# Kernel optimization log

Hardware: AMD Instinct MI355X
Metric: run time of the kernel (lower is better)

Reference implementation:

```python
import jax, jax.numpy as jnp
import numpy as np

EPS = 1e-09


def _glorot(key, shape):
    fan_in, fan_out = shape[-2], shape[-1]
    std = (2.0 / (fan_in + fan_out)) ** 0.5
    return jax.random.normal(key, shape, dtype=jnp.float32) * std


def setup_inputs() -> dict:
    key = jax.random.key(0)
    kx, k1, k2, k3, k4 = jax.random.split(key, 5)
    B, S, D = 2, 1024, 256
    H, K = 8, 32  # key_dim_frac = 1/8
    return {
        "x": jax.random.normal(kx, (B, S, D), dtype=jnp.float32),
        "Wks": _glorot(k1, (H, D, K)),
        "Wqs": _glorot(k2, (H, D, K)),
        "Wvs": _glorot(k3, (H, D, D)),
        "Wo": _glorot(k4, (H, D, D)),
    }


def reference(x, Wks, Wqs, Wvs, Wo):
    # Per-head projections: [H, B, S, K] / [H, B, S, D]
    keys = jnp.einsum('bsd,hdk->hbsk', x, Wks)
    queries = jnp.einsum('bsd,hdk->hbsk', x, Wqs)
    values = jnp.einsum('bsd,hde->hbse', x, Wvs)

    # Feature map: elu + 1 (strictly positive)
    keys = jax.nn.elu(keys) + 1.0
    queries = jax.nn.elu(queries) + 1.0

    # Auxiliary pairwise attention map [H, B, S, S], causal-masked, row-normalized
    att = jnp.einsum('hbsk,hbtk->hbst', queries, keys)
    S = att.shape[-1]
    causal = jnp.tril(jnp.ones((S, S), dtype=att.dtype))
    att = att * causal
    att = att / (jnp.sum(att, axis=-1, keepdims=True) + EPS)

    # Causal linear attention via cumulative sums of outer products
    # [H, B, S, D, K] cumulative state (memory-bound, mirrors tf.cumsum)
    kv = jnp.einsum('hbsk,hbsd->hbsdk', keys, values)
    kv_cum = jnp.cumsum(kv, axis=2)
    numerator = jnp.einsum('hbsdk,hbsk->hbsd', kv_cum, queries)
    denominator = jnp.einsum('hbsk,hbsk->hbs', jnp.cumsum(keys, axis=2), queries)
    node = numerator / (denominator[..., None] + EPS)

    # Output projection, summed over heads: [B, S, D]
    out = jnp.einsum('hbsd,hde->bse', node, Wo)
    return (out, att)
```

## Files before the change

### kernel.cpp

```cpp
#include <hip/hip_runtime.h>
#include <hip/hip_bf16.h>
#include <cstdio>

#define PB 2
#define PS 1024
#define PD 256
#define PK 32
#define PH 8
#define HB (PH*PB)
#define BS (PB*PS)
#define EPS 1e-9f

typedef __attribute__((ext_vector_type(8))) short bf16x8;
typedef __attribute__((ext_vector_type(4))) float f32x4;

__device__ inline unsigned short f2bf(float f) {
    __hip_bfloat16 h = __float2bfloat16(f);
    return *reinterpret_cast<unsigned short*>(&h);
}

__global__ void k_xb(const float* __restrict__ x, unsigned short* __restrict__ xb) {
    int i = blockIdx.x*256 + threadIdx.x;
    float4 v = ((const float4*)x)[i];
    ushort4 o = {f2bf(v.x), f2bf(v.y), f2bf(v.z), f2bf(v.w)};
    ((ushort4*)xb)[i] = o;
}

__global__ void k_transpose_qk(const float* __restrict__ Wqs, const float* __restrict__ Wks,
                               unsigned short* __restrict__ WqT, unsigned short* __restrict__ WkT) {
    int h = blockIdx.x;
    const float* S = (blockIdx.y ? Wks : Wqs) + (size_t)h*8192;
    unsigned short* D = (blockIdx.y ? WkT : WqT) + (size_t)h*8192;
    __shared__ float T[256*33];
    int tid = threadIdx.x;
#pragma unroll
    for (int p = 0; p < 32; ++p) {
        int idx = p*256 + tid;
        T[(idx>>5)*33 + (idx&31)] = S[idx];
    }
    __syncthreads();
#pragma unroll
    for (int p = 0; p < 8; ++p) {
        int o4 = p*256 + tid;
        int kk = o4 >> 6, d = (o4 & 63)*4;
        ushort4 o;
        o.x = f2bf(T[(d+0)*33 + kk]); o.y = f2bf(T[(d+1)*33 + kk]);
        o.z = f2bf(T[(d+2)*33 + kk]); o.w = f2bf(T[(d+3)*33 + kk]);
        *(ushort4*)(D + (size_t)kk*256 + d) = o;
    }
}

__global__ void k_transpose256(const float* __restrict__ src, unsigned short* __restrict__ dst,
                               int dst_row_stride, int dst_head_stride) {
    int e0 = blockIdx.x*64, d0 = blockIdx.y*64, h = blockIdx.z;
    __shared__ float T[64][69];
    const float* S = src + (size_t)h*65536;
    int ty = threadIdx.x>>4, c4 = threadIdx.x&15;
#pragma unroll
    for (int p = 0; p < 4; ++p) {
        int r = p*16 + ty;
        float4 v = *(const float4*)(S + (size_t)(d0+r)*256 + e0 + c4*4);
        T[r][c4*4+0]=v.x; T[r][c4*4+1]=v.y; T[r][c4*4+2]=v.z; T[r][c4*4+3]=v.w;
    }
    __syncthreads();
    unsigned short* D = dst + (size_t)h*dst_head_stride;
#pragma unroll
    for (int p = 0; p < 4; ++p) {
        int er = p*16 + ty;
        ushort4 o;
        o.x = f2bf(T[c4*4+0][er]); o.y = f2bf(T[c4*4+1][er]);
        o.z = f2bf(T[c4*4+2][er]); o.w = f2bf(T[c4*4+3][er]);
        *(ushort4*)(D + (size_t)(e0+er)*dst_row_stride + d0 + c4*4) = o;
    }
}

__global__ __launch_bounds__(256) void k_proj_qk_mfma(
    const unsigned short* __restrict__ xb, const unsigned short* __restrict__ WqT,
    const unsigned short* __restrict__ WkT,
    float* __restrict__ Q, float* __restrict__ Kf,
    unsigned short* __restrict__ Qb, unsigned short* __restrict__ Kb)
{
    int m0 = blockIdx.x*64;
    int isK = blockIdx.y;
    int n0 = blockIdx.z*64;
    const unsigned short* W = isK ? WkT : WqT;
    int tid = threadIdx.x, w = tid>>6, l15 = tid&15, g = (tid>>4)&3;
    f32x4 zf = {0.f,0.f,0.f,0.f};
    f32x4 acc[4] = {zf,zf,zf,zf};
    const unsigned short* arow = xb + (size_t)(m0+16*w+l15)*256 + 8*g;
#pragma unroll
    for (int kk = 0; kk < 8; ++kk) {
        bf16x8 af = *(const bf16x8*)(arow + kk*32);
#pragma unroll
        for (int nt = 0; nt < 4; ++nt) {
            bf16x8 bf = *(const bf16x8*)(W + (size_t)(n0+16*nt+l15)*256 + kk*32 + 8*g);
            acc[nt] = __builtin_amdgcn_mfma_f32_16x16x32_bf16(af, bf, acc[nt], 0, 0, 0);
        }
    }
    int bs_base = m0 + 16*w + 4*g;
#pragma unroll
    for (int nt = 0; nt < 4; ++nt) {
        int col = n0 + 16*nt + l15;
        int h = col>>5, kk = col&31;
#pragma unroll
        for (int j = 0; j < 4; ++j) {
            int bs = bs_base + j;
            int b = bs>>10, s = bs&1023;
            float z = acc[nt][j];
            z = z > 0.f ? z + 1.f : expf(z);
            size_t idx = ((size_t)(h*PB+b)*PS + s)*PK + kk;
            if (isK) { Kf[idx] = z; Kb[idx] = f2bf(z); }
            else     { Q[idx]  = z; Qb[idx] = f2bf(z); }
        }
    }
}

__global__ void k_cumsum(const float* __restrict__ Kf, float* __restrict__ cumK) {
    int hb  = blockIdx.x;
    int tid = threadIdx.x;
    int c = tid >> 5, kk = tid & 31;
    const float* src = Kf   + hb*(PS*PK) + c*128*PK + kk;
    float*       dst = cumK + hb*(PS*PK) + c*128*PK + kk;
    float sum = 0.f;
#pragma unroll 8
    for (int i = 0; i < 128; ++i) sum += src[i*PK];
    __shared__ float ssum[8][32];
    ssum[c][kk] = sum;
    __syncthreads();
    float acc = 0.f;
    for (int j = 0; j < c; ++j) acc += ssum[j][kk];
#pragma unroll 8
    for (int i = 0; i < 128; ++i) { acc += src[i*PK]; dst[i*PK] = acc; }
}

__global__ void k_den(const float* __restrict__ Q, const float* __restrict__ cumK,
                      float* __restrict__ den) {
    int i = blockIdx.x*256 + threadIdx.x;
    const float4* q  = (const float4*)(Q    + (size_t)i*PK);
    const float4* ck = (const float4*)(cumK + (size_t)i*PK);
    float acc = 0.f;
#pragma unroll
    for (int j = 0; j < 8; ++j) {
        float4 a = q[j], b = ck[j];
        acc += a.x*b.x + a.y*b.y + a.z*b.z + a.w*b.w;
    }
    den[i] = acc + EPS;
}

__global__ __launch_bounds__(256) void k_proj_v_mfma(
    const unsigned short* __restrict__ xb, const unsigned short* __restrict__ WvT,
    unsigned short* __restrict__ Vt)
{
    int e0 = blockIdx.x*64, m0 = blockIdx.y*64, h = blockIdx.z;
    int tid = threadIdx.x, w = tid>>6, l15 = tid&15, g = (tid>>4)&3;
    f32x4 zf = {0.f,0.f,0.f,0.f};
    f32x4 acc[4] = {zf,zf,zf,zf};
    const unsigned short* arow = xb + (size_t)(m0+16*w+l15)*256 + 8*g;
    const unsigned short* Wb = WvT + (size_t)h*65536;
#pragma unroll
    for (int kk = 0; kk < 8; ++kk) {
        bf16x8 af = *(const bf16x8*)(arow + kk*32);
#pragma unroll
        for (int nt = 0; nt < 4; ++nt) {
            bf16x8 bf = *(const bf16x8*)(Wb + (size_t)(e0+16*nt+l15)*256 + kk*32 + 8*g);
            acc[nt] = __builtin_amdgcn_mfma_f32_16x16x32_bf16(af, bf, acc[nt], 0, 0, 0);
        }
    }
    unsigned short* VtT = Vt + ((size_t)h*32 + blockIdx.y)*(256*64);
#pragma unroll
    for (int nt = 0; nt < 4; ++nt) {
        ushort4 o = {f2bf(acc[nt][0]), f2bf(acc[nt][1]), f2bf(acc[nt][2]), f2bf(acc[nt][3])};
        *(ushort4*)(VtT + (size_t)(e0+16*nt+l15)*64 + 16*w + 4*g) = o;
    }
}

__global__ void k_att_zero(float* __restrict__ att) {
    int st = blockIdx.x;
    int hb = blockIdx.y;
    int s0 = st * 64;
    int c0 = s0 + 64;
    int nz4 = (PS - c0) >> 2;
    float* base = att + (size_t)hb*PS*PS + (size_t)s0*PS + c0;
    int r = threadIdx.x >> 2;
    int l4 = threadIdx.x & 3;
    float4 z = {0.f, 0.f, 0.f, 0.f};
    for (int c4 = l4; c4 < nz4; c4 += 4)
        *(float4*)(base + (size_t)r*PS + c4*4) = z;
}

__global__ __launch_bounds__(256) void k_att_low(
    const unsigned short* __restrict__ Qb, const unsigned short* __restrict__ Kb,
    const float* __restrict__ den, float* __restrict__ att)
{
    int tt = blockIdx.x, st = blockIdx.y, hb = blockIdx.z;
    if (tt >= st) return;
    int s0 = st*64, t0 = tt*64;
    int tid = threadIdx.x, w = tid>>6, l15 = tid&15, g = (tid>>4)&3;
    f32x4 zf = {0.f,0.f,0.f,0.f};
    bf16x8 qf = *(const bf16x8*)(Qb + ((size_t)hb*PS + s0 + 16*w + l15)*PK + 8*g);
    f32x4 p[4];
#pragma unroll
    for (int nt = 0; nt < 4; ++nt) {
        bf16x8 kf = *(const bf16x8*)(Kb + ((size_t)hb*PS + t0 + 16*nt + l15)*PK + 8*g);
        p[nt] = __builtin_amdgcn_mfma_f32_16x16x32_bf16(qf, kf, zf, 0, 0, 0);
    }
    float* attb = att + (size_t)hb*PS*PS;
    float rd[4];
#pragma unroll
    for (int j = 0; j < 4; ++j) rd[j] = 1.0f / den[hb*PS + s0 + 16*w + 4*g + j];
#pragma unroll
    for (int nt = 0; nt < 4; ++nt)
#pragma unroll
        for (int j = 0; j < 4; ++j)
            attb[(size_t)(s0 + 16*w + 4*g + j)*PS + t0 + 16*nt + l15] = p[nt][j] * rd[j];
}

__global__ __launch_bounds__(256) void k_kv_sums(
    const unsigned short* __restrict__ Kb, const unsigned short* __restrict__ Vt,
    float* __restrict__ KVs)
{
    int c = blockIdx.x, hb = blockIdx.y;
    int tid = threadIdx.x, w = tid>>6, l15 = tid&15, g = (tid>>4)&3;
    __shared__ unsigned short KT[32*72];
#pragma unroll
    for (int i = 0; i < 8; ++i) {
        int flat = tid + i*256;
        KT[(flat&31)*72 + (flat>>5)] = Kb[((size_t)hb*PS + c*64 + (flat>>5))*PK + (flat&31)];
    }
    __syncthreads();
    const unsigned short* Vtt = Vt + ((size_t)hb*16 + c)*(256*64);
    f32x4 zf = {0.f,0.f,0.f,0.f};
    f32x4 acc[4][2];
#pragma unroll
    for (int mt = 0; mt < 4; ++mt) { acc[mt][0] = zf; acc[mt][1] = zf; }
#pragma unroll
    for (int ks = 0; ks < 2; ++ks) {
        bf16x8 af[4];
#pragma unroll
        for (int mt = 0; mt < 4; ++mt)
            af[mt] = *(const bf16x8*)(Vtt + (size_t)(64*w + 16*mt + l15)*64 + 32*ks + 8*g);
#pragma unroll
        for (int nt = 0; nt < 2; ++nt) {
            bf16x8 bf = *(const bf16x8*)(KT + (16*nt + l15)*72 + 32*ks + 8*g);
#pragma unroll
            for (int mt = 0; mt < 4; ++mt)
                acc[mt][nt] = __builtin_amdgcn_mfma_f32_16x16x32_bf16(af[mt], bf, acc[mt][nt], 0, 0, 0);
        }
    }
    float* o = KVs + ((size_t)hb*16 + c)*8192;
#pragma unroll
    for (int mt = 0; mt < 4; ++mt)
#pragma unroll
        for (int nt = 0; nt < 2; ++nt)
#pragma unroll
            for (int j = 0; j < 4; ++j)
                o[(size_t)(64*w + 16*mt + 4*g + j)*32 + 16*nt + l15] = acc[mt][nt][j];
}

__global__ void k_kv_scan(const float* __restrict__ KVs, unsigned short* __restrict__ KVpre) {
    int hb = blockIdx.y;
    int i = blockIdx.x*256 + threadIdx.x;
    const float* src = KVs + (size_t)hb*16*8192 + i;
    unsigned short* dst = KVpre + (size_t)hb*16*8192 + i;
    float acc = 0.f;
#pragma unroll
    for (int c = 0; c < 16; ++c) { dst[c*8192] = f2bf(acc); acc += src[c*8192]; }
}

__global__ __launch_bounds__(256) void k_node(
    const unsigned short* __restrict__ Qb, const unsigned short* __restrict__ Kb,
    const float* __restrict__ den, const unsigned short* __restrict__ Vt,
    const unsigned short* __restrict__ KVpre,
    float* __restrict__ att, unsigned short* __restrict__ nodeB)
{
    int c = blockIdx.x, hb = blockIdx.y;
    int s0 = c*64;
    int tid = threadIdx.x, w = tid>>6, l15 = tid&15, g = (tid>>4)&3;
    __shared__ unsigned short PL[64*72];
    __shared__ float rden[64];
    if (tid < 64) rden[tid] = 1.0f / den[hb*PS + s0 + tid];

    f32x4 zf = {0.f,0.f,0.f,0.f};
    bf16x8 qf = *(const bf16x8*)(Qb + ((size_t)hb*PS + s0 + 16*w + l15)*PK + 8*g);

    const unsigned short* KVp = KVpre + ((size_t)hb*16 + c)*8192;
    f32x4 acc[16];
#pragma unroll
    for (int nt = 0; nt < 16; ++nt) {
        bf16x8 bf = *(const bf16x8*)(KVp + (size_t)(16*nt + l15)*32 + 8*g);
        acc[nt] = __builtin_amdgcn_mfma_f32_16x16x32_bf16(qf, bf, zf, 0, 0, 0);
    }
    f32x4 p[4];
#pragma unroll
    for (int nt4 = 0; nt4 < 4; ++nt4) {
        bf16x8 kf = *(const bf16x8*)(Kb + ((size_t)hb*PS + s0 + 16*nt4 + l15)*PK + 8*g);
        p[nt4] = __builtin_amdgcn_mfma_f32_16x16x32_bf16(qf, kf, zf, 0, 0, 0);
    }
    __syncthreads();
    float* attb = att + (size_t)hb*PS*PS;
#pragma unroll
    for (int nt4 = 0; nt4 < 4; ++nt4) {
#pragma unroll
        for (int j = 0; j < 4; ++j) {
            int r = 16*w + 4*g + j;
            int tc = 16*nt4 + l15;
            float v = p[nt4][j] * rden[r];
            if (tc > r) v = 0.f;
            attb[(size_t)(s0 + r)*PS + s0 + tc] = v;
            PL[r*72 + tc] = f2bf(v);
        }
    }
#pragma unroll
    for (int nt = 0; nt < 16; ++nt)
#pragma unroll
        for (int j = 0; j < 4; ++j)
            acc[nt][j] *= rden[16*w + 4*g + j];
    __syncthreads();
    const unsigned short* Vtt = Vt + ((size_t)hb*16 + c)*(256*64);
#pragma unroll
    for (int ks = 0; ks < 2; ++ks) {
        bf16x8 af = *(const bf16x8*)(PL + (size_t)(16*w + l15)*72 + 32*ks + 8*g);
#pragma unroll
        for (int nt = 0; nt < 16; ++nt) {
            bf16x8 vf = *(const bf16x8*)(Vtt + (size_t)(16*nt + l15)*64 + 32*ks + 8*g);
            acc[nt] = __builtin_amdgcn_mfma_f32_16x16x32_bf16(af, vf, acc[nt], 0, 0, 0);
        }
    }
    int h = hb >> 1, b = hb & 1;
    unsigned short* np = nodeB + ((size_t)(b*PS + s0))*2048 + h*256;
#pragma unroll
    for (int nt = 0; nt < 16; ++nt)
#pragma unroll
        for (int j = 0; j < 4; ++j)
            np[(size_t)(16*w + 4*g + j)*2048 + 16*nt + l15] = f2bf(acc[nt][j]);
}

__global__ __launch_bounds__(256) void k_out2(
    const unsigned short* __restrict__ nodeB, const unsigned short* __restrict__ WoT,
    float* __restrict__ out)
{
    int e0 = blockIdx.x*64, m0 = blockIdx.y*16;
    int tid = threadIdx.x, w = tid>>6, l15 = tid&15, g = (tid>>4)&3;
    f32x4 zf = {0.f,0.f,0.f,0.f};
    f32x4 acc = zf;
    const unsigned short* arow = nodeB + (size_t)(m0 + l15)*2048 + 8*g;
    const unsigned short* brow = WoT + (size_t)(e0 + 16*w + l15)*2048 + 8*g;
#pragma unroll 8
    for (int kk = 0; kk < 64; ++kk) {
        bf16x8 af = *(const bf16x8*)(arow + kk*32);
        bf16x8 bf = *(const bf16x8*)(brow + kk*32);
        acc = __builtin_amdgcn_mfma_f32_16x16x32_bf16(af, bf, acc, 0, 0, 0);
    }
#pragma unroll
    for (int j = 0; j < 4; ++j)
        out[(size_t)(m0 + 4*g + j)*PD + e0 + 16*w + l15] = acc[j];
}

extern "C" void kernel_launch(void* const* d_in, const int* in_sizes, int n_in,
                              void* d_out, int out_size, void* d_ws, size_t ws_size,
                              hipStream_t stream) {
    const float* x   = (const float*)d_in[0];
    const float* Wks = (const float*)d_in[1];
    const float* Wqs = (const float*)d_in[2];
    const float* Wvs = (const float*)d_in[3];
    const float* Wo  = (const float*)d_in[4];

    float* out = (float*)d_out;
    float* att = (float*)d_out + (size_t)PB*PS*PD;

    float* ws = (float*)d_ws;
    float*          Q     = ws + 0;
    float*          Kf    = ws + 524288;
    float*          cumK  = ws + 1048576;
    float*          KVs   = ws + 0;
    float*          den   = ws + 2097152;
    unsigned short* Qb    = (unsigned short*)(ws + 2113536);
    unsigned short* Kb    = (unsigned short*)(ws + 2375680);
    unsigned short* Vt    = (unsigned short*)(ws + 2637824);
    unsigned short* xb    = (unsigned short*)(ws + 4734976);
    unsigned short* WqT   = (unsigned short*)(ws + 4997120);
    unsigned short* WkT   = (unsigned short*)(ws + 5029888);
    unsigned short* WvT   = (unsigned short*)(ws + 5062656);
    unsigned short* WoT   = (unsigned short*)(ws + 5324800);
    unsigned short* nodeB = (unsigned short*)(ws + 5586944);
    unsigned short* KVpre = (unsigned short*)(ws + 7684096);
    const size_t needed = (size_t)8732672 * 4;
    if (ws_size < needed) {
        fprintf(stderr, "kernel_launch: ws_size %zu < needed %zu\n", ws_size, needed);
        return;
    }

    k_xb<<<512, 256, 0, stream>>>(x, xb);
    k_transpose_qk<<<dim3(PH, 2), 256, 0, stream>>>(Wqs, Wks, WqT, WkT);
    k_transpose256<<<dim3(4, 4, PH), 256, 0, stream>>>(Wvs, WvT, 256, 65536);
    k_transpose256<<<dim3(4, 4, PH), 256, 0, stream>>>(Wo,  WoT, 2048, 256);
    k_proj_qk_mfma<<<dim3(32, 2, 4), 256, 0, stream>>>(xb, WqT, WkT, Q, Kf, Qb, Kb);
    k_cumsum<<<HB, 256, 0, stream>>>(Kf, cumK);
    k_den<<<64, 256, 0, stream>>>(Q, cumK, den);
    k_proj_v_mfma<<<dim3(4, 32, PH), 256, 0, stream>>>(xb, WvT, Vt);
    k_att_zero<<<dim3(15, HB), 256, 0, stream>>>(att);
    k_att_low<<<dim3(16, 16, HB), 256, 0, stream>>>(Qb, Kb, den, att);
    k_kv_sums<<<dim3(16, HB), 256, 0, stream>>>(Kb, Vt, KVs);
    k_kv_scan<<<dim3(32, HB), 256, 0, stream>>>(KVs, KVpre);
    k_node<<<dim3(16, HB), 256, 0, stream>>>(Qb, Kb, den, Vt, KVpre, att, nodeB);
    k_out2<<<dim3(4, 128), 256, 0, stream>>>(nodeB, WoT, out);
}
```

Before: 126.3 us.

## Merge prep, projection, cumsum/den and attention kernels into fewer launches

Combines the x cast and the four weight transposes into one prep kernel, and the Q/K and V projections into one MFMA kernel. Fuses the K cumulative sum with the denominator dot product, which now uses wave shuffles and drops the fp32 Q/K/cumK buffers in favour of the bf16 copies. Attention gets one block per row tile that zeroes the upper region, loops over the lower tiles and stages results through shared memory for coalesced float4 stores. Fewer launches and less intermediate traffic come at the cost of much less parallelism in the attention kernel (256 blocks with unbalanced work) and lower precision in the denominator.

```diff
diff --git a/kernel.cpp b/kernel.cpp
--- a/kernel.cpp
+++ b/kernel.cpp
@@ -18,76 +18,91 @@
     __hip_bfloat16 h = __float2bfloat16(f);
     return *reinterpret_cast<unsigned short*>(&h);
 }
-
-__global__ void k_xb(const float* __restrict__ x, unsigned short* __restrict__ xb) {
-    int i = blockIdx.x*256 + threadIdx.x;
-    float4 v = ((const float4*)x)[i];
-    ushort4 o = {f2bf(v.x), f2bf(v.y), f2bf(v.z), f2bf(v.w)};
-    ((ushort4*)xb)[i] = o;
-}
-
-__global__ void k_transpose_qk(const float* __restrict__ Wqs, const float* __restrict__ Wks,
-                               unsigned short* __restrict__ WqT, unsigned short* __restrict__ WkT) {
-    int h = blockIdx.x;
-    const float* S = (blockIdx.y ? Wks : Wqs) + (size_t)h*8192;
-    unsigned short* D = (blockIdx.y ? WkT : WqT) + (size_t)h*8192;
-    __shared__ float T[256*33];
-    int tid = threadIdx.x;
-#pragma unroll
-    for (int p = 0; p < 32; ++p) {
-        int idx = p*256 + tid;
-        T[(idx>>5)*33 + (idx&31)] = S[idx];
-    }
-    __syncthreads();
-#pragma unroll
-    for (int p = 0; p < 8; ++p) {
-        int o4 = p*256 + tid;
-        int kk = o4 >> 6, d = (o4 & 63)*4;
-        ushort4 o;
-        o.x = f2bf(T[(d+0)*33 + kk]); o.y = f2bf(T[(d+1)*33 + kk]);
-        o.z = f2bf(T[(d+2)*33 + kk]); o.w = f2bf(T[(d+3)*33 + kk]);
-        *(ushort4*)(D + (size_t)kk*256 + d) = o;
-    }
-}
-
-__global__ void k_transpose256(const float* __restrict__ src, unsigned short* __restrict__ dst,
-                               int dst_row_stride, int dst_head_stride) {
-    int e0 = blockIdx.x*64, d0 = blockIdx.y*64, h = blockIdx.z;
-    __shared__ float T[64][69];
-    const float* S = src + (size_t)h*65536;
-    int ty = threadIdx.x>>4, c4 = threadIdx.x&15;
+__device__ inline float bf2f(unsigned short u) {
+    return __bfloat162float(*reinterpret_cast<__hip_bfloat16*>(&u));
+}
+
+__global__ __launch_bounds__(256) void k_prep(
+    const float* __restrict__ x, const float* __restrict__ Wqs,
+    const float* __restrict__ Wks, const float* __restrict__ Wvs,
+    const float* __restrict__ Wo,
+    unsigned short* __restrict__ xb, unsigned short* __restrict__ WqT,
+    unsigned short* __restrict__ WkT, unsigned short* __restrict__ WvT,
+    unsigned short* __restrict__ WoT)
+{
+    __shared__ float smem[8448];
+    int bid = blockIdx.x, tid = threadIdx.x;
+    if (bid < 512) {
+        int i = bid*256 + tid;
+        float4 v = ((const float4*)x)[i];
+        ushort4 o = {f2bf(v.x), f2bf(v.y), f2bf(v.z), f2bf(v.w)};
+        ((ushort4*)xb)[i] = o;
+        return;
+    }
+    if (bid < 528) {
+        int r2 = bid - 512;
+        int h = r2 >> 1, isK = r2 & 1;
+        const float* S = (isK ? Wks : Wqs) + (size_t)h*8192;
+        unsigned short* D = (isK ? WkT : WqT) + (size_t)h*8192;
+#pragma unroll
+        for (int p = 0; p < 32; ++p) {
+            int idx = p*256 + tid;
+            smem[(idx>>5)*33 + (idx&31)] = S[idx];
+        }
+        __syncthreads();
+#pragma unroll
+        for (int p = 0; p < 8; ++p) {
+            int o4 = p*256 + tid;
+            int kk = o4 >> 6, d = (o4 & 63)*4;
+            ushort4 o;
+            o.x = f2bf(smem[(d+0)*33 + kk]); o.y = f2bf(smem[(d+1)*33 + kk]);
+            o.z = f2bf(smem[(d+2)*33 + kk]); o.w = f2bf(smem[(d+3)*33 + kk]);
+            *(ushort4*)(D + (size_t)kk*256 + d) = o;
+        }
+        return;
+    }
+    int r3 = bid - 528;
+    const float* S; unsigned short* dst; int rs, hs;
+    if (r3 < 128) { S = Wvs; dst = WvT; rs = 256;  hs = 65536; }
+    else          { r3 -= 128; S = Wo; dst = WoT; rs = 2048; hs = 256; }
+    int e0 = (r3 & 3)*64, d0 = ((r3>>2) & 3)*64, h = r3 >> 4;
+    float (*T)[69] = (float(*)[69])smem;
+    const float* Sh = S + (size_t)h*65536;
+    int ty = tid>>4, c4 = tid&15;
 #pragma unroll
     for (int p = 0; p < 4; ++p) {
         int r = p*16 + ty;
-        float4 v = *(const float4*)(S + (size_t)(d0+r)*256 + e0 + c4*4);
+        float4 v = *(const float4*)(Sh + (size_t)(d0+r)*256 + e0 + c4*4);
         T[r][c4*4+0]=v.x; T[r][c4*4+1]=v.y; T[r][c4*4+2]=v.z; T[r][c4*4+3]=v.w;
     }
     __syncthreads();
-    unsigned short* D = dst + (size_t)h*dst_head_stride;
+    unsigned short* D = dst + (size_t)h*hs;
 #pragma unroll
     for (int p = 0; p < 4; ++p) {
         int er = p*16 + ty;
         ushort4 o;
         o.x = f2bf(T[c4*4+0][er]); o.y = f2bf(T[c4*4+1][er]);
         o.z = f2bf(T[c4*4+2][er]); o.w = f2bf(T[c4*4+3][er]);
-        *(ushort4*)(D + (size_t)(e0+er)*dst_row_stride + d0 + c4*4) = o;
-    }
-}
-
-__global__ __launch_bounds__(256) void k_proj_qk_mfma(
+        *(ushort4*)(D + (size_t)(e0+er)*rs + d0 + c4*4) = o;
+    }
+}
+
+__global__ __launch_bounds__(256) void k_proj(
     const unsigned short* __restrict__ xb, const unsigned short* __restrict__ WqT,
-    const unsigned short* __restrict__ WkT,
-    float* __restrict__ Q, float* __restrict__ Kf,
-    unsigned short* __restrict__ Qb, unsigned short* __restrict__ Kb)
-{
-    int m0 = blockIdx.x*64;
-    int isK = blockIdx.y;
-    int n0 = blockIdx.z*64;
-    const unsigned short* W = isK ? WkT : WqT;
+    const unsigned short* __restrict__ WkT, const unsigned short* __restrict__ WvT,
+    unsigned short* __restrict__ Qb, unsigned short* __restrict__ Kb,
+    unsigned short* __restrict__ Vt)
+{
+    int z = blockIdx.z;
+    int m0 = blockIdx.y*64, n0 = blockIdx.x*64;
     int tid = threadIdx.x, w = tid>>6, l15 = tid&15, g = (tid>>4)&3;
     f32x4 zf = {0.f,0.f,0.f,0.f};
     f32x4 acc[4] = {zf,zf,zf,zf};
     const unsigned short* arow = xb + (size_t)(m0+16*w+l15)*256 + 8*g;
+    const unsigned short* W;
+    if (z < 8)       W = WvT + (size_t)z*65536;
+    else if (z == 8) W = WqT;
+    else             W = WkT;
 #pragma unroll
     for (int kk = 0; kk < 8; ++kk) {
         bf16x8 af = *(const bf16x8*)(arow + kk*32);
@@ -97,122 +112,113 @@
             acc[nt] = __builtin_amdgcn_mfma_f32_16x16x32_bf16(af, bf, acc[nt], 0, 0, 0);
         }
     }
-    int bs_base = m0 + 16*w + 4*g;
-#pragma unroll
-    for (int nt = 0; nt < 4; ++nt) {
-        int col = n0 + 16*nt + l15;
-        int h = col>>5, kk = col&31;
-#pragma unroll
-        for (int j = 0; j < 4; ++j) {
-            int bs = bs_base + j;
-            int b = bs>>10, s = bs&1023;
-            float z = acc[nt][j];
-            z = z > 0.f ? z + 1.f : expf(z);
-            size_t idx = ((size_t)(h*PB+b)*PS + s)*PK + kk;
-            if (isK) { Kf[idx] = z; Kb[idx] = f2bf(z); }
-            else     { Q[idx]  = z; Qb[idx] = f2bf(z); }
-        }
-    }
-}
-
-__global__ void k_cumsum(const float* __restrict__ Kf, float* __restrict__ cumK) {
+    if (z < 8) {
+        unsigned short* VtT = Vt + ((size_t)z*32 + blockIdx.y)*(256*64);
+#pragma unroll
+        for (int nt = 0; nt < 4; ++nt) {
+            ushort4 o = {f2bf(acc[nt][0]), f2bf(acc[nt][1]), f2bf(acc[nt][2]), f2bf(acc[nt][3])};
+            *(ushort4*)(VtT + (size_t)(n0+16*nt+l15)*64 + 16*w + 4*g) = o;
+        }
+    } else {
+        unsigned short* dst = (z == 8) ? Qb : Kb;
+        int bs_base = m0 + 16*w + 4*g;
+#pragma unroll
+        for (int nt = 0; nt < 4; ++nt) {
+            int col = n0 + 16*nt + l15;
+            int h = col>>5, kk = col&31;
+#pragma unroll
+            for (int j = 0; j < 4; ++j) {
+                int bs = bs_base + j;
+                int b = bs>>10, s = bs&1023;
+                float zv = acc[nt][j];
+                zv = zv > 0.f ? zv + 1.f : expf(zv);
+                dst[((size_t)(h*PB+b)*PS + s)*PK + kk] = f2bf(zv);
+            }
+        }
+    }
+}
+
+__global__ void k_cumden(const unsigned short* __restrict__ Qb,
+                         const unsigned short* __restrict__ Kb,
+                         float* __restrict__ den) {
     int hb  = blockIdx.x;
     int tid = threadIdx.x;
     int c = tid >> 5, kk = tid & 31;
-    const float* src = Kf   + hb*(PS*PK) + c*128*PK + kk;
-    float*       dst = cumK + hb*(PS*PK) + c*128*PK + kk;
+    size_t base = (size_t)hb*(PS*PK) + (size_t)c*128*PK + kk;
     float sum = 0.f;
 #pragma unroll 8
-    for (int i = 0; i < 128; ++i) sum += src[i*PK];
+    for (int i = 0; i < 128; ++i) sum += bf2f(Kb[base + i*PK]);
     __shared__ float ssum[8][32];
     ssum[c][kk] = sum;
     __syncthreads();
     float acc = 0.f;
     for (int j = 0; j < c; ++j) acc += ssum[j][kk];
-#pragma unroll 8
-    for (int i = 0; i < 128; ++i) { acc += src[i*PK]; dst[i*PK] = acc; }
-}
-
-__global__ void k_den(const float* __restrict__ Q, const float* __restrict__ cumK,
-                      float* __restrict__ den) {
-    int i = blockIdx.x*256 + threadIdx.x;
-    const float4* q  = (const float4*)(Q    + (size_t)i*PK);
-    const float4* ck = (const float4*)(cumK + (size_t)i*PK);
-    float acc = 0.f;
-#pragma unroll
-    for (int j = 0; j < 8; ++j) {
-        float4 a = q[j], b = ck[j];
-        acc += a.x*b.x + a.y*b.y + a.z*b.z + a.w*b.w;
-    }
-    den[i] = acc + EPS;
-}
-
-__global__ __launch_bounds__(256) void k_proj_v_mfma(
-    const unsigned short* __restrict__ xb, const unsigned short* __restrict__ WvT,
-    unsigned short* __restrict__ Vt)
-{
-    int e0 = blockIdx.x*64, m0 = blockIdx.y*64, h = blockIdx.z;
-    int tid = threadIdx.x, w = tid>>6, l15 = tid&15, g = (tid>>4)&3;
-    f32x4 zf = {0.f,0.f,0.f,0.f};
-    f32x4 acc[4] = {zf,zf,zf,zf};
-    const unsigned short* arow = xb + (size_t)(m0+16*w+l15)*256 + 8*g;
-    const unsigned short* Wb = WvT + (size_t)h*65536;
-#pragma unroll
-    for (int kk = 0; kk < 8; ++kk) {
-        bf16x8 af = *(const bf16x8*)(arow + kk*32);
-#pragma unroll
-        for (int nt = 0; nt < 4; ++nt) {
-            bf16x8 bf = *(const bf16x8*)(Wb + (size_t)(e0+16*nt+l15)*256 + kk*32 + 8*g);
-            acc[nt] = __builtin_amdgcn_mfma_f32_16x16x32_bf16(af, bf, acc[nt], 0, 0, 0);
-        }
-    }
-    unsigned short* VtT = Vt + ((size_t)h*32 + blockIdx.y)*(256*64);
-#pragma unroll
-    for (int nt = 0; nt < 4; ++nt) {
-        ushort4 o = {f2bf(acc[nt][0]), f2bf(acc[nt][1]), f2bf(acc[nt][2]), f2bf(acc[nt][3])};
-        *(ushort4*)(VtT + (size_t)(e0+16*nt+l15)*64 + 16*w + 4*g) = o;
-    }
-}
-
-__global__ void k_att_zero(float* __restrict__ att) {
-    int st = blockIdx.x;
-    int hb = blockIdx.y;
-    int s0 = st * 64;
-    int c0 = s0 + 64;
-    int nz4 = (PS - c0) >> 2;
-    float* base = att + (size_t)hb*PS*PS + (size_t)s0*PS + c0;
-    int r = threadIdx.x >> 2;
-    int l4 = threadIdx.x & 3;
-    float4 z = {0.f, 0.f, 0.f, 0.f};
-    for (int c4 = l4; c4 < nz4; c4 += 4)
-        *(float4*)(base + (size_t)r*PS + c4*4) = z;
-}
-
-__global__ __launch_bounds__(256) void k_att_low(
+#pragma unroll 4
+    for (int i = 0; i < 128; ++i) {
+        acc += bf2f(Kb[base + i*PK]);
+        float t = bf2f(Qb[base + i*PK]) * acc;
+        t += __shfl_xor(t, 1);  t += __shfl_xor(t, 2);
+        t += __shfl_xor(t, 4);  t += __shfl_xor(t, 8);
+        t += __shfl_xor(t, 16);
+        if (kk == 0) den[hb*PS + c*128 + i] = t + EPS;
+    }
+}
+
+__global__ __launch_bounds__(256) void k_att(
     const unsigned short* __restrict__ Qb, const unsigned short* __restrict__ Kb,
     const float* __restrict__ den, float* __restrict__ att)
 {
-    int tt = blockIdx.x, st = blockIdx.y, hb = blockIdx.z;
-    if (tt >= st) return;
-    int s0 = st*64, t0 = tt*64;
+    int st = blockIdx.x, hb = blockIdx.y;
+    int s0 = st*64;
     int tid = threadIdx.x, w = tid>>6, l15 = tid&15, g = (tid>>4)&3;
+
+    alignas(16) __shared__ float PT[64][68];
+    __shared__ float rden[64];
+
+    float* attb = att + (size_t)hb*PS*PS;
+    int c0 = s0 + 64;
+    int nzf4 = (PS - c0) >> 2;
+    if (nzf4 > 0 && tid < nzf4) {
+        float4 z = {0.f,0.f,0.f,0.f};
+        float* zb = attb + (size_t)s0*PS + c0 + tid*4;
+#pragma unroll 4
+        for (int r = 0; r < 64; ++r)
+            *(float4*)(zb + (size_t)r*PS) = z;
+    }
+    if (tid < 64) rden[tid] = 1.0f / den[hb*PS + s0 + tid];
+
+    if (st == 0) return;
+
+    bf16x8 qf = *(const bf16x8*)(Qb + ((size_t)hb*PS + s0 + 16*w + l15)*PK + 8*g);
     f32x4 zf = {0.f,0.f,0.f,0.f};
-    bf16x8 qf = *(const bf16x8*)(Qb + ((size_t)hb*PS + s0 + 16*w + l15)*PK + 8*g);
-    f32x4 p[4];
-#pragma unroll
-    for (int nt = 0; nt < 4; ++nt) {
-        bf16x8 kf = *(const bf16x8*)(Kb + ((size_t)hb*PS + t0 + 16*nt + l15)*PK + 8*g);
-        p[nt] = __builtin_amdgcn_mfma_f32_16x16x32_bf16(qf, kf, zf, 0, 0, 0);
-    }
-    float* attb = att + (size_t)hb*PS*PS;
+    __syncthreads();
     float rd[4];
 #pragma unroll
-    for (int j = 0; j < 4; ++j) rd[j] = 1.0f / den[hb*PS + s0 + 16*w + 4*g + j];
-#pragma unroll
-    for (int nt = 0; nt < 4; ++nt)
-#pragma unroll
-        for (int j = 0; j < 4; ++j)
-            attb[(size_t)(s0 + 16*w + 4*g + j)*PS + t0 + 16*nt + l15] = p[nt][j] * rd[j];
+    for (int j = 0; j < 4; ++j) rd[j] = rden[16*w + 4*g + j];
+
+    for (int tt = 0; tt < st; ++tt) {
+        int t0 = tt*64;
+        f32x4 p[4];
+#pragma unroll
+        for (int nt = 0; nt < 4; ++nt) {
+            bf16x8 kf = *(const bf16x8*)(Kb + ((size_t)hb*PS + t0 + 16*nt + l15)*PK + 8*g);
+            p[nt] = __builtin_amdgcn_mfma_f32_16x16x32_bf16(qf, kf, zf, 0, 0, 0);
+        }
+#pragma unroll
+        for (int nt = 0; nt < 4; ++nt)
+#pragma unroll
+            for (int j = 0; j < 4; ++j)
+                PT[16*w + 4*g + j][16*nt + l15] = p[nt][j] * rd[j];
+        __syncthreads();
+#pragma unroll
+        for (int pp = 0; pp < 4; ++pp) {
+            int f4 = tid + pp*256;
+            int r = f4 >> 4, c4 = f4 & 15;
+            float4 v = *(const float4*)&PT[r][c4*4];
+            *(float4*)(attb + (size_t)(s0+r)*PS + t0 + c4*4) = v;
+        }
+        __syncthreads();
+    }
 }
 
 __global__ __launch_bounds__(256) void k_kv_sums(
@@ -369,20 +375,17 @@
     float* att = (float*)d_out + (size_t)PB*PS*PD;
 
     float* ws = (float*)d_ws;
-    float*          Q     = ws + 0;
-    float*          Kf    = ws + 524288;
-    float*          cumK  = ws + 1048576;
-    float*          KVs   = ws + 0;
-    float*          den   = ws + 2097152;
-    unsigned short* Qb    = (unsigned short*)(ws + 2113536);
-    unsigned short* Kb    = (unsigned short*)(ws + 2375680);
-    unsigned short* Vt    = (unsigned short*)(ws + 2637824);
-    unsigned short* xb    = (unsigned short*)(ws + 4734976);
-    unsigned short* WqT   = (unsigned short*)(ws + 4997120);
-    unsigned short* WkT   = (unsigned short*)(ws + 5029888);
-    unsigned short* WvT   = (unsigned short*)(ws + 5062656);
-    unsigned short* WoT   = (unsigned short*)(ws + 5324800);
-    unsigned short* nodeB = (unsigned short*)(ws + 5586944);
+    float*          den   = ws + 0;
+    unsigned short* Qb    = (unsigned short*)(ws + 16384);
+    unsigned short* Kb    = (unsigned short*)(ws + 278528);
+    unsigned short* Vt    = (unsigned short*)(ws + 540672);
+    unsigned short* xb    = (unsigned short*)(ws + 2637824);
+    unsigned short* WqT   = (unsigned short*)(ws + 2899968);
+    unsigned short* WkT   = (unsigned short*)(ws + 2932736);
+    unsigned short* WvT   = (unsigned short*)(ws + 2965504);
+    unsigned short* WoT   = (unsigned short*)(ws + 3227648);
+    unsigned short* nodeB = (unsigned short*)(ws + 3489792);
+    float*          KVs   = ws + 5586944;
     unsigned short* KVpre = (unsigned short*)(ws + 7684096);
     const size_t needed = (size_t)8732672 * 4;
     if (ws_size < needed) {
@@ -390,16 +393,10 @@
         return;
     }
 
-    k_xb<<<512, 256, 0, stream>>>(x, xb);
-    k_transpose_qk<<<dim3(PH, 2), 256, 0, stream>>>(Wqs, Wks, WqT, WkT);
-    k_transpose256<<<dim3(4, 4, PH), 256, 0, stream>>>(Wvs, WvT, 256, 65536);
-    k_transpose256<<<dim3(4, 4, PH), 256, 0, stream>>>(Wo,  WoT, 2048, 256);
-    k_proj_qk_mfma<<<dim3(32, 2, 4), 256, 0, stream>>>(xb, WqT, WkT, Q, Kf, Qb, Kb);
-    k_cumsum<<<HB, 256, 0, stream>>>(Kf, cumK);
-    k_den<<<64, 256, 0, stream>>>(Q, cumK, den);
-    k_proj_v_mfma<<<dim3(4, 32, PH), 256, 0, stream>>>(xb, WvT, Vt);
-    k_att_zero<<<dim3(15, HB), 256, 0, stream>>>(att);
-    k_att_low<<<dim3(16, 16, HB), 256, 0, stream>>>(Qb, Kb, den, att);
+    k_prep<<<784, 256, 0, stream>>>(x, Wqs, Wks, Wvs, Wo, xb, WqT, WkT, WvT, WoT);
+    k_proj<<<dim3(4, 32, 10), 256, 0, stream>>>(xb, WqT, WkT, WvT, Qb, Kb, Vt);
+    k_cumden<<<HB, 256, 0, stream>>>(Qb, Kb, den);
+    k_att<<<dim3(16, HB), 256, 0, stream>>>(Qb, Kb, den, att);
     k_kv_sums<<<dim3(16, HB), 256, 0, stream>>>(Kb, Vt, KVs);
     k_kv_scan<<<dim3(32, HB), 256, 0, stream>>>(KVs, KVpre);
     k_node<<<dim3(16, HB), 256, 0, stream>>>(Qb, Kb, den, Vt, KVpre, att, nodeB);
```

Result: slower. 154.1 us (+22.0%).
